# Optimization experiments

Measured on AMD Instinct MI355X. Metric: run time of the kernel, lower is better.

The kernel has to match this reference:

```python
import jax, jax.numpy as jnp
import numpy as np

N = 1024
C = 50000
D = 128
M_MARGIN = 0.35
S_SCALE = 30.0
LAMDA = 0.01


def setup_inputs() -> dict:
    key = jax.random.key(0)
    k1, k2, k3 = jax.random.split(key, 3)
    feature = jax.random.normal(k1, (N, D), dtype=jnp.float32)
    weight = jax.random.normal(k2, (C, D), dtype=jnp.float32)
    label = jax.random.randint(k3, (N,), 0, C, dtype=jnp.int64)
    return {"feature": feature, "weight": weight, "label": label}


def reference(feature, weight, label):
    eps = 1e-8  # torch CosineSimilarity eps
    f = feature / jnp.maximum(jnp.linalg.norm(feature, axis=-1, keepdims=True), eps)
    w = weight / jnp.maximum(jnp.linalg.norm(weight, axis=-1, keepdims=True), eps)
    cos = jnp.einsum("nd,cd->nc", f, w)  # [N, C] cosine similarities
    onehot = jax.nn.one_hot(label, C, dtype=cos.dtype)  # [N, C]
    # CosFace: subtract margin m from the target-class cosine, scale by s
    logits = S_SCALE * (cos - M_MARGIN * onehot)
    target_logit = S_SCALE * (jnp.take_along_axis(cos, label[:, None], axis=1)[:, 0] - M_MARGIN)
    # -log( exp(t) / (exp(t) + sum_{j != y} exp(s*cos_j)) ) = logsumexp(logits) - t
    lse = jax.nn.logsumexp(logits, axis=-1)  # [N]
    loss_lmc = jnp.mean(lse - target_logit)
    # center loss: 0.5 * sum_i ||f_i - w_{y_i}||^2
    diff = feature - weight[label]
    loss_c = 0.5 * jnp.sum(diff * diff)
    return loss_lmc + LAMDA * loss_c
```

## Files before the change

### kernel.cpp

```cpp
#include <hip/hip_runtime.h>

#define N_ROWS   1024
#define D_DIM    128
#define C_CLS    50000
#define C_PAD    50048
#define NCT      391
#define NG       64
#define S_SCALE  30.0f
#define M_MARGIN 0.35f

typedef short s8v __attribute__((ext_vector_type(8)));
typedef float f4v __attribute__((ext_vector_type(4)));

__device__ inline unsigned short f2bf(float f) {
    unsigned u = __float_as_uint(f);
    u += 0x7FFF + ((u >> 16) & 1);
    return (unsigned short)(u >> 16);
}
__device__ inline float bf2f(unsigned short h) {
    return __uint_as_float(((unsigned)h) << 16);
}
__device__ inline void load_lds16(const char* src, unsigned char* lds) {
    __builtin_amdgcn_global_load_lds(
        (const __attribute__((address_space(1))) void*)src,
        (__attribute__((address_space(3))) void*)lds, 16, 0, 0);
}

__global__ void norm_rows_fused(const float* __restrict__ weight,
                                const float* __restrict__ feature,
                                unsigned short* __restrict__ what,
                                unsigned short* __restrict__ fhat) {
    int wid = threadIdx.x >> 6, lane = threadIdx.x & 63;
    int r = blockIdx.x * 4 + wid;
    const float* src;
    unsigned short* dst;
    int srcRow, valid;
    if (r < C_PAD) {
        src = weight; dst = what; srcRow = r; valid = (r < C_CLS);
    } else {
        src = feature; dst = fhat; srcRow = r - C_PAD; valid = 1;
    }
    float2 v = make_float2(0.f, 0.f);
    if (valid) v = ((const float2*)src)[(size_t)srcRow * 64 + lane];
    float ss = v.x * v.x + v.y * v.y;
    #pragma unroll
    for (int s = 1; s < 64; s <<= 1) ss += __shfl_xor(ss, s, 64);
    float inv = valid ? 1.0f / fmaxf(sqrtf(ss), 1e-8f) : 0.f;
    int dstRow = (r < C_PAD) ? r : srcRow;
    ((ushort2*)dst)[(size_t)dstRow * 64 + lane] =
        make_ushort2(f2bf(v.x * inv), f2bf(v.y * inv));
}

__global__ __launch_bounds__(256, 2)
void gemm_exp_kernel(const short* __restrict__ fhat,
                     const short* __restrict__ what,
                     float* __restrict__ part2) {
    __shared__ __align__(16) unsigned char smem[65536];
    const int g   = blockIdx.x;
    const int rt  = blockIdx.y;
    const int tid = threadIdx.x;
    const int wid = tid >> 6;
    const int lane = tid & 63;
    const int nt = (g < 7) ? 7 : 6;

    const char* aSrc  = (const char*)fhat + (size_t)rt * 32768;
    const char* bBase = (const char*)what;

    #pragma unroll
    for (int i = 0; i < 8; i++) {
        int o = wid * 8192 + i * 1024 + lane * 16;
        int s = o ^ (((o >> 8) & 7) << 4);
        load_lds16(aSrc + s, smem + o);
        load_lds16(bBase + (size_t)g * 32768 + s, smem + 32768 + o);
    }
    __syncthreads();

    const int wr = (wid >> 1) * 64;
    const int wc = (wid & 1) * 64;
    const int lrow = lane & 15;
    const int kgrp = lane >> 4;

    s8v afr[4][4];
    #pragma unroll
    for (int kk = 0; kk < 4; kk++)
        #pragma unroll
        for (int m = 0; m < 4; m++) {
            int row = wr + m * 16 + lrow;
            int b = (row * 256 + kk * 64 + kgrp * 16) ^ ((row & 7) << 4);
            afr[kk][m] = *(const s8v*)(smem + b);
        }
    __syncthreads();

    float esum[4][4];
    #pragma unroll
    for (int m = 0; m < 4; m++)
        #pragma unroll
        for (int j = 0; j < 4; j++) esum[m][j] = 0.f;

    int cur = 1;
    for (int t = 0; t < nt; ++t) {
        const int ct = g + 64 * t;
        if (t + 1 < nt) {
            const char* src = bBase + (size_t)(ct + 64) * 32768;
            unsigned char* dstb = smem + (cur ^ 1) * 32768;
            #pragma unroll
            for (int i = 0; i < 8; i++) {
                int o = wid * 8192 + i * 1024 + lane * 16;
                int s = o ^ (((o >> 8) & 7) << 4);
                load_lds16(src + s, dstb + o);
            }
        }

        const unsigned char* bb = smem + cur * 32768;
        f4v acc[4][4];
        f4v zero = {0.f, 0.f, 0.f, 0.f};
        #pragma unroll
        for (int m = 0; m < 4; m++)
            #pragma unroll
            for (int n = 0; n < 4; n++) acc[m][n] = zero;

        #pragma unroll
        for (int kk = 0; kk < 4; kk++) {
            s8v bfr[4];
            #pragma unroll
            for (int n = 0; n < 4; n++) {
                int row = wc + n * 16 + lrow;
                int b = (row * 256 + kk * 64 + kgrp * 16) ^ ((row & 7) << 4);
                bfr[n] = *(const s8v*)(bb + b);
            }
            #pragma unroll
            for (int m = 0; m < 4; m++)
                #pragma unroll
                for (int n = 0; n < 4; n++)
                    acc[m][n] = __builtin_amdgcn_mfma_f32_16x16x32_bf16(
                        afr[kk][m], bfr[n], acc[m][n], 0, 0, 0);
        }

        if (ct != NCT - 1) {
            #pragma unroll
            for (int m = 0; m < 4; m++)
                #pragma unroll
                for (int n = 0; n < 4; n++)
                    #pragma unroll
                    for (int j = 0; j < 4; j++)
                        esum[m][j] += __expf(S_SCALE * acc[m][n][j]);
        } else {
            int cbase = ct * 128 + wc;
            #pragma unroll
            for (int m = 0; m < 4; m++)
                #pragma unroll
                for (int n = 0; n < 4; n++) {
                    int gc = cbase + n * 16 + lrow;
                    #pragma unroll
                    for (int j = 0; j < 4; j++)
                        if (gc < C_CLS) esum[m][j] += __expf(S_SCALE * acc[m][n][j]);
                }
        }
        __syncthreads();
        cur ^= 1;
    }

    float* srow = (float*)smem;
    #pragma unroll
    for (int m = 0; m < 4; m++)
        #pragma unroll
        for (int j = 0; j < 4; j++) {
            float v = esum[m][j];
            v += __shfl_xor(v, 1, 64);
            v += __shfl_xor(v, 2, 64);
            v += __shfl_xor(v, 4, 64);
            v += __shfl_xor(v, 8, 64);
            if (lrow == 0)
                srow[(wid & 1) * 128 + wr + m * 16 + kgrp * 4 + j] = v;
        }
    __syncthreads();
    if (tid < 128)
        part2[(size_t)(rt * 128 + tid) * NG + g] = srow[tid] + srow[128 + tid];
}

__global__ void finalize_rows_kernel(const float* __restrict__ part2,
                                     const unsigned short* __restrict__ fhat,
                                     const unsigned short* __restrict__ what,
                                     const float* __restrict__ feature,
                                     const float* __restrict__ weight,
                                     const int* __restrict__ label,
                                     float* __restrict__ rowval) {
    int wid = threadIdx.x >> 6, lane = threadIdx.x & 63;
    int n = blockIdx.x * 4 + wid;
    int y = label[n];

    float S = part2[(size_t)n * NG + lane];

    float2 f2 = ((const float2*)feature)[(size_t)n * 64 + lane];
    float2 w2 = ((const float2*)weight)[(size_t)y * 64 + lane];
    float dx = f2.x - w2.x, dy = f2.y - w2.y;
    float cl = dx * dx + dy * dy;

    ushort2 fh = ((const ushort2*)fhat)[(size_t)n * 64 + lane];
    ushort2 wh = ((const ushort2*)what)[(size_t)y * 64 + lane];
    float cy = bf2f(fh.x) * bf2f(wh.x) + bf2f(fh.y) * bf2f(wh.y);

    #pragma unroll
    for (int s = 1; s < 64; s <<= 1) {
        S  += __shfl_xor(S, s, 64);
        cl += __shfl_xor(cl, s, 64);
        cy += __shfl_xor(cy, s, 64);
    }
    if (lane == 0) {
        float t  = S_SCALE * (cy - M_MARGIN);
        float Sp = S - __expf(S_SCALE * cy) + __expf(t);
        rowval[n] = (logf(Sp) - t) * (1.0f / (float)N_ROWS) + 0.005f * cl;
    }
}

__global__ void reduce_final_kernel(const float* __restrict__ rowval, float* __restrict__ out) {
    __shared__ float sbuf[4];
    int t = threadIdx.x;
    float v = rowval[t] + rowval[t + 256] + rowval[t + 512] + rowval[t + 768];
    #pragma unroll
    for (int s = 1; s < 64; s <<= 1) v += __shfl_xor(v, s, 64);
    if ((t & 63) == 0) sbuf[t >> 6] = v;
    __syncthreads();
    if (t == 0) out[0] = sbuf[0] + sbuf[1] + sbuf[2] + sbuf[3];
}

extern "C" void kernel_launch(void* const* d_in, const int* in_sizes, int n_in,
                              void* d_out, int out_size, void* d_ws, size_t ws_size,
                              hipStream_t stream) {
    const float* feature = (const float*)d_in[0];
    const float* weight  = (const float*)d_in[1];
    const int*   label   = (const int*)d_in[2];

    const size_t WS_NEEDED = 13340672;
    if (ws_size < WS_NEEDED) return;

    char* ws = (char*)d_ws;
    unsigned short* what = (unsigned short*)ws;
    unsigned short* fhat = (unsigned short*)(ws + 12812288);
    float*         part2 = (float*)(ws + 13074432);
    float*        rowval = (float*)(ws + 13336576);

    norm_rows_fused<<<dim3((C_PAD + N_ROWS) / 4), 256, 0, stream>>>(weight, feature, what, fhat);
    gemm_exp_kernel<<<dim3(NG, 8), 256, 0, stream>>>((const short*)fhat, (const short*)what, part2);
    finalize_rows_kernel<<<dim3(N_ROWS / 4), 256, 0, stream>>>(part2, fhat, what, feature, weight,
                                                               label, rowval);
    reduce_final_kernel<<<1, 256, 0, stream>>>(rowval, (float*)d_out);
}
```

Baseline: 39.60 us.

## Halve GEMM class tile to 64, double grid, raise occupancy, use exp2

The fused cosine-GEMM/exp kernel now processes 64-class tiles with each wave owning 32 rows, cutting LDS to 32KB and register footprint so four blocks per CU can be resident, and the grid doubles to 128 class groups. Per-wave partial sums are written directly to global memory, with no LDS cross-wave reduction, and finalize sums two 64-wide partial halves. The exp is replaced by a raw exp2 with a prescaled constant to save a multiply per element. In exchange, each block reuses less data per B load and the partial buffer grows.

Result: faster. 37.81 us (-4.5%).

```diff
diff --git a/kernel.cpp b/kernel.cpp
--- a/kernel.cpp
+++ b/kernel.cpp
@@ -4,10 +4,11 @@
 #define D_DIM    128
 #define C_CLS    50000
 #define C_PAD    50048
-#define NCT      391
-#define NG       64
+#define NCT64    782
+#define NG       128
 #define S_SCALE  30.0f
 #define M_MARGIN 0.35f
+#define EXP2_SCALE 43.2808512266689f
 
 typedef short s8v __attribute__((ext_vector_type(8)));
 typedef float f4v __attribute__((ext_vector_type(4)));
@@ -46,22 +47,21 @@
     #pragma unroll
     for (int s = 1; s < 64; s <<= 1) ss += __shfl_xor(ss, s, 64);
     float inv = valid ? 1.0f / fmaxf(sqrtf(ss), 1e-8f) : 0.f;
-    int dstRow = (r < C_PAD) ? r : srcRow;
-    ((ushort2*)dst)[(size_t)dstRow * 64 + lane] =
+    ((ushort2*)dst)[(size_t)srcRow * 64 + lane] =
         make_ushort2(f2bf(v.x * inv), f2bf(v.y * inv));
 }
 
-__global__ __launch_bounds__(256, 2)
+__global__ __launch_bounds__(256, 4)
 void gemm_exp_kernel(const short* __restrict__ fhat,
                      const short* __restrict__ what,
                      float* __restrict__ part2) {
-    __shared__ __align__(16) unsigned char smem[65536];
+    __shared__ __align__(16) unsigned char smem[32768];
     const int g   = blockIdx.x;
     const int rt  = blockIdx.y;
     const int tid = threadIdx.x;
     const int wid = tid >> 6;
     const int lane = tid & 63;
-    const int nt = (g < 7) ? 7 : 6;
+    const int nt = (g < 14) ? 7 : 6;
 
     const char* aSrc  = (const char*)fhat + (size_t)rt * 32768;
     const char* bBase = (const char*)what;
@@ -71,51 +71,59 @@
         int o = wid * 8192 + i * 1024 + lane * 16;
         int s = o ^ (((o >> 8) & 7) << 4);
         load_lds16(aSrc + s, smem + o);
-        load_lds16(bBase + (size_t)g * 32768 + s, smem + 32768 + o);
-    }
-    __syncthreads();
-
-    const int wr = (wid >> 1) * 64;
-    const int wc = (wid & 1) * 64;
+    }
+    __syncthreads();
+
     const int lrow = lane & 15;
     const int kgrp = lane >> 4;
 
-    s8v afr[4][4];
+    s8v afr[4][2];
     #pragma unroll
     for (int kk = 0; kk < 4; kk++)
         #pragma unroll
-        for (int m = 0; m < 4; m++) {
-            int row = wr + m * 16 + lrow;
+        for (int m = 0; m < 2; m++) {
+            int row = wid * 32 + m * 16 + lrow;
             int b = (row * 256 + kk * 64 + kgrp * 16) ^ ((row & 7) << 4);
             afr[kk][m] = *(const s8v*)(smem + b);
         }
     __syncthreads();
 
-    float esum[4][4];
-    #pragma unroll
-    for (int m = 0; m < 4; m++)
+    {
+        const char* src = bBase + (size_t)g * 16384;
+        #pragma unroll
+        for (int i = 0; i < 4; i++) {
+            int o = wid * 4096 + i * 1024 + lane * 16;
+            int s = o ^ (((o >> 8) & 7) << 4);
+            load_lds16(src + s, smem + o);
+        }
+    }
+    __syncthreads();
+
+    float esum[2][4];
+    #pragma unroll
+    for (int m = 0; m < 2; m++)
         #pragma unroll
         for (int j = 0; j < 4; j++) esum[m][j] = 0.f;
 
-    int cur = 1;
+    int cur = 0;
     for (int t = 0; t < nt; ++t) {
-        const int ct = g + 64 * t;
+        const int ct = g + 128 * t;
         if (t + 1 < nt) {
-            const char* src = bBase + (size_t)(ct + 64) * 32768;
-            unsigned char* dstb = smem + (cur ^ 1) * 32768;
-            #pragma unroll
-            for (int i = 0; i < 8; i++) {
-                int o = wid * 8192 + i * 1024 + lane * 16;
+            const char* src = bBase + (size_t)(ct + 128) * 16384;
+            unsigned char* dstb = smem + (cur ^ 1) * 16384;
+            #pragma unroll
+            for (int i = 0; i < 4; i++) {
+                int o = wid * 4096 + i * 1024 + lane * 16;
                 int s = o ^ (((o >> 8) & 7) << 4);
                 load_lds16(src + s, dstb + o);
             }
         }
 
-        const unsigned char* bb = smem + cur * 32768;
-        f4v acc[4][4];
+        const unsigned char* bb = smem + cur * 16384;
+        f4v acc[2][4];
         f4v zero = {0.f, 0.f, 0.f, 0.f};
         #pragma unroll
-        for (int m = 0; m < 4; m++)
+        for (int m = 0; m < 2; m++)
             #pragma unroll
             for (int n = 0; n < 4; n++) acc[m][n] = zero;
 
@@ -124,45 +132,45 @@
             s8v bfr[4];
             #pragma unroll
             for (int n = 0; n < 4; n++) {
-                int row = wc + n * 16 + lrow;
+                int row = n * 16 + lrow;
                 int b = (row * 256 + kk * 64 + kgrp * 16) ^ ((row & 7) << 4);
                 bfr[n] = *(const s8v*)(bb + b);
             }
             #pragma unroll
-            for (int m = 0; m < 4; m++)
+            for (int m = 0; m < 2; m++)
                 #pragma unroll
                 for (int n = 0; n < 4; n++)
                     acc[m][n] = __builtin_amdgcn_mfma_f32_16x16x32_bf16(
                         afr[kk][m], bfr[n], acc[m][n], 0, 0, 0);
         }
 
-        if (ct != NCT - 1) {
-            #pragma unroll
-            for (int m = 0; m < 4; m++)
+        if (ct != NCT64 - 1) {
+            #pragma unroll
+            for (int m = 0; m < 2; m++)
                 #pragma unroll
                 for (int n = 0; n < 4; n++)
                     #pragma unroll
                     for (int j = 0; j < 4; j++)
-                        esum[m][j] += __expf(S_SCALE * acc[m][n][j]);
+                        esum[m][j] += __builtin_amdgcn_exp2f(EXP2_SCALE * acc[m][n][j]);
         } else {
-            int cbase = ct * 128 + wc;
-            #pragma unroll
-            for (int m = 0; m < 4; m++)
+            int cbase = ct * 64;
+            #pragma unroll
+            for (int m = 0; m < 2; m++)
                 #pragma unroll
                 for (int n = 0; n < 4; n++) {
                     int gc = cbase + n * 16 + lrow;
                     #pragma unroll
                     for (int j = 0; j < 4; j++)
-                        if (gc < C_CLS) esum[m][j] += __expf(S_SCALE * acc[m][n][j]);
+                        if (gc < C_CLS)
+                            esum[m][j] += __builtin_amdgcn_exp2f(EXP2_SCALE * acc[m][n][j]);
                 }
         }
         __syncthreads();
         cur ^= 1;
     }
 
-    float* srow = (float*)smem;
-    #pragma unroll
-    for (int m = 0; m < 4; m++)
+    #pragma unroll
+    for (int m = 0; m < 2; m++)
         #pragma unroll
         for (int j = 0; j < 4; j++) {
             float v = esum[m][j];
@@ -170,12 +178,11 @@
             v += __shfl_xor(v, 2, 64);
             v += __shfl_xor(v, 4, 64);
             v += __shfl_xor(v, 8, 64);
-            if (lrow == 0)
-                srow[(wid & 1) * 128 + wr + m * 16 + kgrp * 4 + j] = v;
-        }
-    __syncthreads();
-    if (tid < 128)
-        part2[(size_t)(rt * 128 + tid) * NG + g] = srow[tid] + srow[128 + tid];
+            if (lrow == 0) {
+                int row = rt * 128 + wid * 32 + m * 16 + kgrp * 4 + j;
+                part2[(size_t)row * NG + g] = v;
+            }
+        }
 }
 
 __global__ void finalize_rows_kernel(const float* __restrict__ part2,
@@ -189,7 +196,7 @@
     int n = blockIdx.x * 4 + wid;
     int y = label[n];
 
-    float S = part2[(size_t)n * NG + lane];
+    float S = part2[(size_t)n * NG + lane] + part2[(size_t)n * NG + 64 + lane];
 
     float2 f2 = ((const float2*)feature)[(size_t)n * 64 + lane];
     float2 w2 = ((const float2*)weight)[(size_t)y * 64 + lane];
@@ -231,14 +238,14 @@
     const float* weight  = (const float*)d_in[1];
     const int*   label   = (const int*)d_in[2];
 
-    const size_t WS_NEEDED = 13340672;
+    const size_t WS_NEEDED = 13602816;
     if (ws_size < WS_NEEDED) return;
 
     char* ws = (char*)d_ws;
     unsigned short* what = (unsigned short*)ws;
     unsigned short* fhat = (unsigned short*)(ws + 12812288);
     float*         part2 = (float*)(ws + 13074432);
-    float*        rowval = (float*)(ws + 13336576);
+    float*        rowval = (float*)(ws + 13598720);
 
     norm_rows_fused<<<dim3((C_PAD + N_ROWS) / 4), 256, 0, stream>>>(weight, feature, what, fhat);
     gemm_exp_kernel<<<dim3(NG, 8), 256, 0, stream>>>((const short*)fhat, (const short*)what, part2);
```

## Drop LDS staging in GEMM-exp kernel, load fragments directly into registers

Applied to the files above, without the earlier changes.

The fused GEMM+exp kernel no longer stages A and B tiles through LDS with global_load_lds and barriers. Each wave now loads its MFMA fragments straight from global memory into registers, double-buffering B across 64-column tiles over 128 column groups. The per-block LDS reduction is replaced by direct per-wave partial-sum writes, with 256 partials per row summed in finalize. The exp is also switched to a raw exp2 with a prescaled constant. This trades LDS traffic and barrier stalls for more uncoalesced global/L2 fragment loads and more register pressure.

New measurement: 54.82 us. 1.38x slower.

```diff
diff --git a/kernel.cpp b/kernel.cpp
--- a/kernel.cpp
+++ b/kernel.cpp
@@ -4,10 +4,12 @@
 #define D_DIM    128
 #define C_CLS    50000
 #define C_PAD    50048
-#define NCT      391
-#define NG       64
+#define NCT64    782
+#define NG       128
+#define NPART    256
 #define S_SCALE  30.0f
 #define M_MARGIN 0.35f
+#define EXP2_SCALE 43.2808512266689f
 
 typedef short s8v __attribute__((ext_vector_type(8)));
 typedef float f4v __attribute__((ext_vector_type(4)));
@@ -19,11 +21,6 @@
 }
 __device__ inline float bf2f(unsigned short h) {
     return __uint_as_float(((unsigned)h) << 16);
-}
-__device__ inline void load_lds16(const char* src, unsigned char* lds) {
-    __builtin_amdgcn_global_load_lds(
-        (const __attribute__((address_space(1))) void*)src,
-        (__attribute__((address_space(3))) void*)lds, 16, 0, 0);
 }
 
 __global__ void norm_rows_fused(const float* __restrict__ weight,
@@ -46,50 +43,84 @@
     #pragma unroll
     for (int s = 1; s < 64; s <<= 1) ss += __shfl_xor(ss, s, 64);
     float inv = valid ? 1.0f / fmaxf(sqrtf(ss), 1e-8f) : 0.f;
-    int dstRow = (r < C_PAD) ? r : srcRow;
-    ((ushort2*)dst)[(size_t)dstRow * 64 + lane] =
+    ((ushort2*)dst)[(size_t)srcRow * 64 + lane] =
         make_ushort2(f2bf(v.x * inv), f2bf(v.y * inv));
+}
+
+__device__ __forceinline__ void loadB(s8v (&B)[8], const char* bRow, int ct) {
+    const char* p = bRow + (size_t)ct * 16384;
+    B[0] = *(const s8v*)(p);
+    B[1] = *(const s8v*)(p + 64);
+    B[2] = *(const s8v*)(p + 128);
+    B[3] = *(const s8v*)(p + 192);
+    B[4] = *(const s8v*)(p + 4096);
+    B[5] = *(const s8v*)(p + 4096 + 64);
+    B[6] = *(const s8v*)(p + 4096 + 128);
+    B[7] = *(const s8v*)(p + 4096 + 192);
+}
+
+__device__ __forceinline__ void computeTile(const s8v (&afr)[4][4], const s8v (&B)[8],
+                                            float (&esum)[4][4], int ct, int colBase) {
+    f4v acc[4][2];
+    f4v zero = {0.f, 0.f, 0.f, 0.f};
+    #pragma unroll
+    for (int m = 0; m < 4; m++) { acc[m][0] = zero; acc[m][1] = zero; }
+
+    #pragma unroll
+    for (int kk = 0; kk < 4; kk++)
+        #pragma unroll
+        for (int m = 0; m < 4; m++) {
+            acc[m][0] = __builtin_amdgcn_mfma_f32_16x16x32_bf16(afr[kk][m], B[kk],     acc[m][0], 0, 0, 0);
+            acc[m][1] = __builtin_amdgcn_mfma_f32_16x16x32_bf16(afr[kk][m], B[4 + kk], acc[m][1], 0, 0, 0);
+        }
+
+    if (ct != NCT64 - 1) {
+        #pragma unroll
+        for (int m = 0; m < 4; m++)
+            #pragma unroll
+            for (int n = 0; n < 2; n++)
+                #pragma unroll
+                for (int j = 0; j < 4; j++)
+                    esum[m][j] += __builtin_amdgcn_exp2f(EXP2_SCALE * acc[m][n][j]);
+    } else {
+        #pragma unroll
+        for (int n = 0; n < 2; n++) {
+            int gc = colBase + n * 16;
+            #pragma unroll
+            for (int m = 0; m < 4; m++)
+                #pragma unroll
+                for (int j = 0; j < 4; j++)
+                    if (gc < C_CLS)
+                        esum[m][j] += __builtin_amdgcn_exp2f(EXP2_SCALE * acc[m][n][j]);
+        }
+    }
 }
 
 __global__ __launch_bounds__(256, 2)
 void gemm_exp_kernel(const short* __restrict__ fhat,
                      const short* __restrict__ what,
                      float* __restrict__ part2) {
-    __shared__ __align__(16) unsigned char smem[65536];
     const int g   = blockIdx.x;
     const int rt  = blockIdx.y;
     const int tid = threadIdx.x;
     const int wid = tid >> 6;
     const int lane = tid & 63;
-    const int nt = (g < 7) ? 7 : 6;
-
-    const char* aSrc  = (const char*)fhat + (size_t)rt * 32768;
-    const char* bBase = (const char*)what;
-
-    #pragma unroll
-    for (int i = 0; i < 8; i++) {
-        int o = wid * 8192 + i * 1024 + lane * 16;
-        int s = o ^ (((o >> 8) & 7) << 4);
-        load_lds16(aSrc + s, smem + o);
-        load_lds16(bBase + (size_t)g * 32768 + s, smem + 32768 + o);
-    }
-    __syncthreads();
-
-    const int wr = (wid >> 1) * 64;
-    const int wc = (wid & 1) * 64;
     const int lrow = lane & 15;
     const int kgrp = lane >> 4;
-
+    const int wrow = wid >> 1;
+    const int wcol = wid & 1;
+    const int nt = (g < 14) ? 7 : 6;
+
+    const char* aBase = (const char*)fhat
+        + ((size_t)(rt * 128 + wrow * 64 + lrow)) * 256 + kgrp * 16;
     s8v afr[4][4];
     #pragma unroll
     for (int kk = 0; kk < 4; kk++)
         #pragma unroll
-        for (int m = 0; m < 4; m++) {
-            int row = wr + m * 16 + lrow;
-            int b = (row * 256 + kk * 64 + kgrp * 16) ^ ((row & 7) << 4);
-            afr[kk][m] = *(const s8v*)(smem + b);
-        }
-    __syncthreads();
+        for (int m = 0; m < 4; m++)
+            afr[kk][m] = *(const s8v*)(aBase + m * 4096 + kk * 64);
+
+    const char* bRow = (const char*)what + ((size_t)(wcol * 32 + lrow)) * 256 + kgrp * 16;
 
     float esum[4][4];
     #pragma unroll
@@ -97,70 +128,22 @@
         #pragma unroll
         for (int j = 0; j < 4; j++) esum[m][j] = 0.f;
 
-    int cur = 1;
-    for (int t = 0; t < nt; ++t) {
-        const int ct = g + 64 * t;
-        if (t + 1 < nt) {
-            const char* src = bBase + (size_t)(ct + 64) * 32768;
-            unsigned char* dstb = smem + (cur ^ 1) * 32768;
-            #pragma unroll
-            for (int i = 0; i < 8; i++) {
-                int o = wid * 8192 + i * 1024 + lane * 16;
-                int s = o ^ (((o >> 8) & 7) << 4);
-                load_lds16(src + s, dstb + o);
-            }
-        }
-
-        const unsigned char* bb = smem + cur * 32768;
-        f4v acc[4][4];
-        f4v zero = {0.f, 0.f, 0.f, 0.f};
-        #pragma unroll
-        for (int m = 0; m < 4; m++)
-            #pragma unroll
-            for (int n = 0; n < 4; n++) acc[m][n] = zero;
-
-        #pragma unroll
-        for (int kk = 0; kk < 4; kk++) {
-            s8v bfr[4];
-            #pragma unroll
-            for (int n = 0; n < 4; n++) {
-                int row = wc + n * 16 + lrow;
-                int b = (row * 256 + kk * 64 + kgrp * 16) ^ ((row & 7) << 4);
-                bfr[n] = *(const s8v*)(bb + b);
-            }
-            #pragma unroll
-            for (int m = 0; m < 4; m++)
-                #pragma unroll
-                for (int n = 0; n < 4; n++)
-                    acc[m][n] = __builtin_amdgcn_mfma_f32_16x16x32_bf16(
-                        afr[kk][m], bfr[n], acc[m][n], 0, 0, 0);
-        }
-
-        if (ct != NCT - 1) {
-            #pragma unroll
-            for (int m = 0; m < 4; m++)
-                #pragma unroll
-                for (int n = 0; n < 4; n++)
-                    #pragma unroll
-                    for (int j = 0; j < 4; j++)
-                        esum[m][j] += __expf(S_SCALE * acc[m][n][j]);
-        } else {
-            int cbase = ct * 128 + wc;
-            #pragma unroll
-            for (int m = 0; m < 4; m++)
-                #pragma unroll
-                for (int n = 0; n < 4; n++) {
-                    int gc = cbase + n * 16 + lrow;
-                    #pragma unroll
-                    for (int j = 0; j < 4; j++)
-                        if (gc < C_CLS) esum[m][j] += __expf(S_SCALE * acc[m][n][j]);
-                }
-        }
-        __syncthreads();
-        cur ^= 1;
-    }
-
-    float* srow = (float*)smem;
+    s8v b0[8], b1[8];
+    int ct = g;
+    const int colBase0 = wcol * 32 + lrow;
+    loadB(b0, bRow, ct);
+    int t = 0;
+    while (true) {
+        if (t + 1 < nt) loadB(b1, bRow, ct + 128);
+        computeTile(afr, b0, esum, ct, ct * 64 + colBase0);
+        if (++t >= nt) break;
+        ct += 128;
+        if (t + 1 < nt) loadB(b0, bRow, ct + 128);
+        computeTile(afr, b1, esum, ct, ct * 64 + colBase0);
+        if (++t >= nt) break;
+        ct += 128;
+    }
+
     #pragma unroll
     for (int m = 0; m < 4; m++)
         #pragma unroll
@@ -170,12 +153,11 @@
             v += __shfl_xor(v, 2, 64);
             v += __shfl_xor(v, 4, 64);
             v += __shfl_xor(v, 8, 64);
-            if (lrow == 0)
-                srow[(wid & 1) * 128 + wr + m * 16 + kgrp * 4 + j] = v;
+            if (lrow == 0) {
+                int row = rt * 128 + wrow * 64 + m * 16 + kgrp * 4 + j;
+                part2[(size_t)row * NPART + g * 2 + wcol] = v;
+            }
         }
-    __syncthreads();
-    if (tid < 128)
-        part2[(size_t)(rt * 128 + tid) * NG + g] = srow[tid] + srow[128 + tid];
 }
 
 __global__ void finalize_rows_kernel(const float* __restrict__ part2,
@@ -189,7 +171,8 @@
     int n = blockIdx.x * 4 + wid;
     int y = label[n];
 
-    float S = part2[(size_t)n * NG + lane];
+    const float* p = part2 + (size_t)n * NPART;
+    float S = p[lane] + p[64 + lane] + p[128 + lane] + p[192 + lane];
 
     float2 f2 = ((const float2*)feature)[(size_t)n * 64 + lane];
     float2 w2 = ((const float2*)weight)[(size_t)y * 64 + lane];
@@ -231,14 +214,14 @@
     const float* weight  = (const float*)d_in[1];
     const int*   label   = (const int*)d_in[2];
 
-    const size_t WS_NEEDED = 13340672;
+    const size_t WS_NEEDED = 14127104;
     if (ws_size < WS_NEEDED) return;
 
     char* ws = (char*)d_ws;
     unsigned short* what = (unsigned short*)ws;
     unsigned short* fhat = (unsigned short*)(ws + 12812288);
     float*         part2 = (float*)(ws + 13074432);
-    float*        rowval = (float*)(ws + 13336576);
+    float*        rowval = (float*)(ws + 14123008);
 
     norm_rows_fused<<<dim3((C_PAD + N_ROWS) / 4), 256, 0, stream>>>(weight, feature, what, fhat);
     gemm_exp_kernel<<<dim3(NG, 8), 256, 0, stream>>>((const short*)fhat, (const short*)what, part2);
```
